# Performance work log

Measured on AMD Instinct MI355X. Metric: run time of the kernel, lower is better.

Reference implementation:

```python
import jax, jax.numpy as jnp
import numpy as np

C_S = 1024
H = 16
M = 1  # num_vector_messages
B, S = 2, 1024
SQRT3 = 3.0 ** 0.5
LN_EPS = 1e-5


def setup_inputs() -> dict:
    key = jax.random.key(0)
    ks = jax.random.split(key, 8)
    s = jax.random.normal(ks[0], (B, S, C_S), dtype=jnp.float32)
    # random proper-ish frames: orthonormalize random 3x3 via QR
    A = jax.random.normal(ks[1], (B, S, 3, 3), dtype=jnp.float32)
    rot, _ = jnp.linalg.qr(A)
    trans = jax.random.normal(ks[2], (B, S, 3), dtype=jnp.float32)
    affine_mask = jnp.ones((B, S), dtype=bool)
    sequence_id = jax.random.randint(ks[3], (B, S), 0, 4, dtype=jnp.int32)
    chain_id = jax.random.randint(ks[4], (B, S), 0, 4, dtype=jnp.int32)
    dim_proj = 4 * H * 3 + H * 3 * M
    ln_w = jnp.ones((C_S,), dtype=jnp.float32)
    w_proj = jax.random.normal(ks[5], (dim_proj, C_S), dtype=jnp.float32) / np.sqrt(C_S)
    w_out = jax.random.normal(ks[6], (C_S, H * 3 * M), dtype=jnp.float32) / np.sqrt(H * 3 * M)
    dist_scale = jnp.zeros((H,), dtype=jnp.float32)
    rot_scale = jnp.zeros((H,), dtype=jnp.float32)
    return {"s": s, "rot": rot, "trans": trans, "ln_w": ln_w, "w_proj": w_proj,
            "w_out": w_out, "dist_scale": dist_scale, "rot_scale": rot_scale,
            "affine_mask": affine_mask, "sequence_id": sequence_id, "chain_id": chain_id}


def reference(s, rot, trans, ln_w, w_proj, w_out, dist_scale, rot_scale,
              affine_mask, sequence_id, chain_id):
    b, n, c = s.shape
    h, m = H, M
    NEG = jnp.finfo(s.dtype).min
    # attention bias: 1.0 for same-sequence pairs, -inf for invalid frames / cross-chain
    seq_eq = (sequence_id[:, :, None] == sequence_id[:, None, :]).astype(s.dtype)
    bias = seq_eq[:, None]  # [b,1,s,s]
    bias = jnp.where(affine_mask[:, None, None, :], bias, NEG)
    chain_diff = chain_id[:, :, None] != chain_id[:, None, :]
    bias = jnp.where(chain_diff[:, None], NEG, bias)
    # LayerNorm (no bias)
    mu = jnp.mean(s, axis=-1, keepdims=True)
    var = jnp.var(s, axis=-1, keepdims=True)
    ns = (s - mu) / jnp.sqrt(var + LN_EPS) * ln_w
    p = jnp.einsum('bsc,dc->bsd', ns, w_proj)
    n_rot = h * 2 * 3 + h * 3 * m
    vec_rot = p[..., :n_rot].reshape(b, n, 2 * h + h * m, 3)
    vec_dist = p[..., n_rot:].reshape(b, n, 2 * h, 3)
    # rotate into global frame; dist vectors also translated
    rot_vecs = jnp.einsum('bsij,bshj->bshi', rot, vec_rot)
    q_rot, k_rot, value = rot_vecs[:, :, :h], rot_vecs[:, :, h:2 * h], rot_vecs[:, :, 2 * h:]
    dist_vecs = jnp.einsum('bsij,bshj->bshi', rot, vec_dist) + trans[:, :, None, :]
    q_dist, k_dist = dist_vecs[:, :, :h], dist_vecs[:, :, h:]
    # distance term [b,h,q,k]
    qd = q_dist.transpose(0, 2, 1, 3)  # b h s 3
    kd = k_dist.transpose(0, 2, 1, 3)
    diff = qd[:, :, :, None, :] - kd[:, :, None, :, :]
    distance_term = jnp.sqrt(jnp.sum(diff * diff, axis=-1)) / SQRT3
    rotation_term = jnp.einsum('bqhd,bkhd->bhqk', q_rot, k_rot) / SQRT3
    dw = jax.nn.softplus(dist_scale)[None, :, None, None]
    rw = jax.nn.softplus(rot_scale)[None, :, None, None]
    attn = rotation_term * rw - distance_term * dw + bias
    attn = jax.nn.softmax(attn, axis=-1)
    # value: b s (h m) 3 -> b h s (m 3)
    v = value.reshape(b, n, h, m, 3).transpose(0, 2, 1, 3, 4).reshape(b, h, n, m * 3)
    out = jnp.einsum('bhqk,bhkd->bhqd', attn, v)
    out = out.reshape(b, h, n, m, 3).transpose(0, 2, 1, 3, 4).reshape(b, n, h * m, 3)
    out = jnp.einsum('bsji,bshj->bshi', rot, out)  # inverse rotation R^T
    out = out.reshape(b, n, h * m * 3)
    out = jnp.where(affine_mask[..., None], out, 0.0)
    return jnp.einsum('bsd,cd->bsc', out, w_out)
```

## Files before the change

### kernel.cpp

```cpp
#include <hip/hip_runtime.h>
#include <math.h>

#define NB 2
#define NS 1024
#define NC 1024
#define NH 16
#define DIMP 240
#define KSPLIT 16
#define AKH 16

constexpr float INV_SQRT3 = 0.57735026919f;
constexpr float LOG2E     = 1.44269504089f;
constexpr float BIAS0     = -23.0831169f;
constexpr float BIAS1     = -21.6404252f;

__global__ __launch_bounds__(256) void pre_kernel(const float* __restrict__ s,
                                                  float2* __restrict__ stats,
                                                  const float* __restrict__ wp,
                                                  float* __restrict__ wt) {
    __shared__ float sh[64 * 61];
    int tid = threadIdx.x;
    if (blockIdx.x < NB * NS / 4) {
        int wave = tid >> 6, lane = tid & 63;
        int row = blockIdx.x * 4 + wave;
        const float4* sp = (const float4*)(s + (size_t)row * NC);
        float sum = 0.0f, sq = 0.0f;
        #pragma unroll
        for (int i = 0; i < 4; i++) {
            float4 v = sp[i * 64 + lane];
            sum += v.x + v.y + v.z + v.w;
            sq  += v.x * v.x + v.y * v.y + v.z * v.z + v.w * v.w;
        }
        #pragma unroll
        for (int off = 32; off; off >>= 1) {
            sum += __shfl_down(sum, off);
            sq  += __shfl_down(sq, off);
        }
        if (lane == 0) {
            float mu  = sum * (1.0f / NC);
            float var = sq * (1.0f / NC) - mu * mu;
            stats[row] = make_float2(mu, rsqrtf(var + 1e-5f));
        }
    } else {
        int bx = blockIdx.x - NB * NS / 4;
        int k0 = (bx & 15) * 64;
        int d0 = (bx >> 4) * 60;
        float (*T)[61] = (float (*)[61])sh;
        #pragma unroll
        for (int i = 0; i < 15; i++) {
            int idx = i * 256 + tid;
            int dd = idx >> 6, kk = idx & 63;
            T[kk][dd] = wp[(size_t)(d0 + dd) * NC + k0 + kk];
        }
        __syncthreads();
        #pragma unroll
        for (int i = 0; i < 15; i++) {
            int idx = i * 256 + tid;
            int kk = idx / 60, dd = idx % 60;
            wt[(size_t)(k0 + kk) * DIMP + d0 + dd] = T[kk][dd];
        }
    }
}

__global__ __launch_bounds__(256) void proj_kernel(const float* __restrict__ s,
                                                   const float2* __restrict__ stats,
                                                   const float* __restrict__ lnw,
                                                   const float* __restrict__ wt,
                                                   float* __restrict__ pp,
                                                   int use_atomic) {
    int tid = threadIdx.x;
    int wave = tid >> 6, lane = tid & 63;
    int row0 = blockIdx.x * 32;
    int ky = blockIdx.y;
    int k0 = ky * 64;

    __shared__ float A[32][64];
    #pragma unroll
    for (int i = 0; i < 2; i++) {
        int idx = tid + i * 256;
        int r = idx >> 4, c4 = idx & 15;
        float4 v = *(const float4*)(s + (size_t)(row0 + r) * NC + k0 + c4 * 4);
        float2 st = stats[row0 + r];
        float4 w = *(const float4*)(lnw + k0 + c4 * 4);
        float4 o;
        o.x = (v.x - st.x) * st.y * w.x;
        o.y = (v.y - st.x) * st.y * w.y;
        o.z = (v.z - st.x) * st.y * w.z;
        o.w = (v.w - st.x) * st.y * w.w;
        *(float4*)&A[r][c4 * 4] = o;
    }
    __syncthreads();

    int wr0 = wave * 8;
    int c0 = lane * 4;
    bool active = c0 < DIMP;
    int c0m = active ? c0 : (DIMP - 4);
    const float* wb = wt + (size_t)k0 * DIMP + c0m;

    float acc[8][4];
    #pragma unroll
    for (int r = 0; r < 8; r++)
        #pragma unroll
        for (int c = 0; c < 4; c++) acc[r][c] = 0.0f;

    float4 wa[4], wx[4];
    #pragma unroll
    for (int j = 0; j < 4; j++) wa[j] = *(const float4*)(wb + (size_t)j * DIMP);

    for (int g = 0; g < 16; g += 2) {
        #pragma unroll
        for (int j = 0; j < 4; j++)
            wx[j] = *(const float4*)(wb + (size_t)((g + 1) * 4 + j) * DIMP);
        #pragma unroll
        for (int r = 0; r < 8; r++) {
            float4 a4 = *(const float4*)&A[wr0 + r][g * 4];
            #pragma unroll
            for (int c = 0; c < 4; c++) {
                float* ac = &acc[r][c];
                *ac = fmaf(a4.x, ((const float*)&wa[0])[c], *ac);
                *ac = fmaf(a4.y, ((const float*)&wa[1])[c], *ac);
                *ac = fmaf(a4.z, ((const float*)&wa[2])[c], *ac);
                *ac = fmaf(a4.w, ((const float*)&wa[3])[c], *ac);
            }
        }
        int kn2 = (g + 2 < 16) ? (g + 2) * 4 : 0;
        #pragma unroll
        for (int j = 0; j < 4; j++)
            wa[j] = *(const float4*)(wb + (size_t)(kn2 + j) * DIMP);
        #pragma unroll
        for (int r = 0; r < 8; r++) {
            float4 a4 = *(const float4*)&A[wr0 + r][(g + 1) * 4];
            #pragma unroll
            for (int c = 0; c < 4; c++) {
                float* ac = &acc[r][c];
                *ac = fmaf(a4.x, ((const float*)&wx[0])[c], *ac);
                *ac = fmaf(a4.y, ((const float*)&wx[1])[c], *ac);
                *ac = fmaf(a4.z, ((const float*)&wx[2])[c], *ac);
                *ac = fmaf(a4.w, ((const float*)&wx[3])[c], *ac);
            }
        }
    }
    if (active) {
        if (use_atomic) {
            #pragma unroll
            for (int r = 0; r < 8; r++)
                #pragma unroll
                for (int c = 0; c < 4; c++)
                    atomicAdd(&pp[(size_t)(row0 + wr0 + r) * DIMP + c0 + c], acc[r][c]);
        } else {
            float* dst = pp + (size_t)ky * (NB * NS * DIMP);
            #pragma unroll
            for (int r = 0; r < 8; r++)
                *(float4*)(dst + (size_t)(row0 + wr0 + r) * DIMP + c0) =
                    make_float4(acc[r][0], acc[r][1], acc[r][2], acc[r][3]);
        }
    }
}

__global__ __launch_bounds__(256) void build_kernel(const float* __restrict__ pp, int nred,
                                                    const float* __restrict__ rot,
                                                    const float* __restrict__ trans,
                                                    const float* __restrict__ dist_scale,
                                                    const float* __restrict__ rot_scale,
                                                    const int* __restrict__ seq,
                                                    const int* __restrict__ chain,
                                                    const int* __restrict__ amask,
                                                    float4* __restrict__ qrb,
                                                    float4* __restrict__ qdb,
                                                    float4* __restrict__ kp) {
    int gid = blockIdx.x * 256 + threadIdx.x;
    if (gid >= NB * NS * 80) return;
    int j  = gid % 80;
    int bs = gid / 80;
    int b  = bs >> 10;
    int si = bs & 1023;
    int off = (j < 48) ? 3 * j : 144 + 3 * (j - 48);
    float vx = 0.0f, vy = 0.0f, vz = 0.0f;
    for (int ky = 0; ky < nred; ky++) {
        const float* pr = pp + (size_t)ky * (NB * NS * DIMP) + (size_t)bs * DIMP + off;
        vx += pr[0]; vy += pr[1]; vz += pr[2];
    }
    const float* R = rot + (size_t)bs * 9;
    float ox = R[0] * vx + R[1] * vy + R[2] * vz;
    float oy = R[3] * vx + R[4] * vy + R[5] * vz;
    float oz = R[6] * vx + R[7] * vy + R[8] * vz;
    if (j >= 48) {
        ox += trans[(size_t)bs * 3 + 0];
        oy += trans[(size_t)bs * 3 + 1];
        oz += trans[(size_t)bs * 3 + 2];
    }
    if (j < 16) {
        float sc = log1pf(__expf(rot_scale[j])) * INV_SQRT3 * LOG2E;
        qrb[(size_t)(b * NH + j) * NS + si] = make_float4(ox * sc, oy * sc, oz * sc, 0.0f);
    } else if (j < 32) {
        int h = j - 16;
        float ck = (float)chain[bs] + 1000.0f * (float)(1 - amask[bs]);
        kp[((size_t)(b * NH + h) * NS + si) * 3 + 0] = make_float4(ox, oy, oz, ck);
    } else if (j < 48) {
        int h = j - 32;
        kp[((size_t)(b * NH + h) * NS + si) * 3 + 2] = make_float4(ox, oy, oz, 0.0f);
    } else if (j < 64) {
        int h = j - 48;
        float sc = log1pf(__expf(dist_scale[h])) * INV_SQRT3 * LOG2E;
        qdb[(size_t)(b * NH + h) * NS + si] = make_float4(ox * sc, oy * sc, oz * sc, 0.0f);
    } else {
        int h = j - 64;
        float sc = log1pf(__expf(dist_scale[h])) * INV_SQRT3 * LOG2E;
        kp[((size_t)(b * NH + h) * NS + si) * 3 + 1] =
            make_float4(ox * sc, oy * sc, oz * sc, (float)seq[bs]);
    }
}

__global__ __launch_bounds__(256) void attn_kernel(
    const float4* __restrict__ qrb, const float4* __restrict__ qdb,
    const float4* __restrict__ kp,
    float4* __restrict__ pacc) {
    __shared__ float4 kS[192];
    int bx = blockIdx.x;
    int ks = bx & (AKH - 1), qc = (bx >> 4) & 3, bh = bx >> 6;
    int tid = threadIdx.x;
    int q = qc * 256 + tid;
    int base = bh * NS;
    const float4* kb = kp + (size_t)base * 3;

    if (tid < 192) kS[tid] = kb[(size_t)ks * 192 + tid];
    __syncthreads();

    float4 a = qrb[base + q];
    float4 d = qdb[base + q];
    float cq = kb[(size_t)q * 3 + 0].w;
    float sq = kb[(size_t)q * 3 + 1].w;

    float l = 0.0f, ax = 0.0f, ay = 0.0f, az = 0.0f;
    #pragma unroll 4
    for (int j = 0; j < 64; j++) {
        float4 f0 = kS[j * 3 + 0];
        float4 f1 = kS[j * 3 + 1];
        float4 f2 = kS[j * 3 + 2];
        float rt = fmaf(a.x, f0.x, fmaf(a.y, f0.y, a.z * f0.z));
        float dx = d.x - f1.x, dy = d.y - f1.y, dz = d.z - f1.z;
        float dist = __builtin_amdgcn_sqrtf(fmaf(dx, dx, fmaf(dy, dy, dz * dz)));
        float dc = f0.w - cq;
        float arg = fmaf(-100.0f, fabsf(dc), rt - dist) +
                    ((f1.w == sq) ? BIAS1 : BIAS0);
        float pw = exp2f(arg);
        l += pw;
        ax = fmaf(pw, f2.x, ax);
        ay = fmaf(pw, f2.y, ay);
        az = fmaf(pw, f2.z, az);
    }
    pacc[(size_t)ks * (32 * NS) + base + q] = make_float4(ax, ay, az, l);
}

__global__ __launch_bounds__(256) void finout_kernel(const float4* __restrict__ pacc,
                                                     const float4* __restrict__ kp,
                                                     const float* __restrict__ rot,
                                                     const float* __restrict__ wout,
                                                     float* __restrict__ out) {
    __shared__ float sm[8][48];
    int tid = threadIdx.x;
    int r0 = blockIdx.x * 8;
    if (tid < 128) {
        int r = tid & 7, h = tid >> 3;
        int bq = r0 + r;
        int b = bq >> 10, q = bq & 1023;
        int i = (b * NH + h) * NS + q;
        float sx = 0.0f, sy = 0.0f, sz = 0.0f, sw = 0.0f;
        #pragma unroll
        for (int j = 0; j < AKH; j++) {
            float4 t = pacc[(size_t)j * (NB * NH * NS) + i];
            sx += t.x; sy += t.y; sz += t.z; sw += t.w;
        }
        float inv = 1.0f / sw;
        float ox = sx * inv, oy = sy * inv, oz = sz * inv;
        const float* R = rot + (size_t)bq * 9;
        float wxv = R[0] * ox + R[3] * oy + R[6] * oz;
        float wyv = R[1] * ox + R[4] * oy + R[7] * oz;
        float wzv = R[2] * ox + R[5] * oy + R[8] * oz;
        float cq = kp[(size_t)i * 3].w;
        if (cq >= 500.0f) { wxv = 0; wyv = 0; wzv = 0; }
        sm[r][h * 3 + 0] = wxv;
        sm[r][h * 3 + 1] = wyv;
        sm[r][h * 3 + 2] = wzv;
    }
    __syncthreads();
    #pragma unroll 1
    for (int ch = 0; ch < 4; ch++) {
        int c = ch * 256 + tid;
        float w[48];
        #pragma unroll
        for (int d = 0; d < 48; d += 4) {
            float4 t = *(const float4*)(wout + (size_t)c * 48 + d);
            w[d] = t.x; w[d + 1] = t.y; w[d + 2] = t.z; w[d + 3] = t.w;
        }
        #pragma unroll 4
        for (int r = 0; r < 8; r++) {
            float acc = 0.0f;
            #pragma unroll
            for (int d = 0; d < 48; d++) acc = fmaf(w[d], sm[r][d], acc);
            out[(size_t)(r0 + r) * NC + c] = acc;
        }
    }
}

extern "C" void kernel_launch(void* const* d_in, const int* in_sizes, int n_in,
                              void* d_out, int out_size, void* d_ws, size_t ws_size,
                              hipStream_t stream) {
    const float* s     = (const float*)d_in[0];
    const float* rot   = (const float*)d_in[1];
    const float* trans = (const float*)d_in[2];
    const float* lnw   = (const float*)d_in[3];
    const float* wproj = (const float*)d_in[4];
    const float* wout  = (const float*)d_in[5];
    const float* dsc   = (const float*)d_in[6];
    const float* rsc   = (const float*)d_in[7];
    const int* amask   = (const int*)d_in[8];
    const int* seq     = (const int*)d_in[9];
    const int* chain   = (const int*)d_in[10];
    float* out = (float*)d_out;

    float2* stats = (float2*)d_ws;
    float4* qrb = (float4*)((float*)d_ws + 4096);
    float4* qdb = qrb + (size_t)NB * NH * NS;
    float4* kpk = qdb + (size_t)NB * NH * NS;
    float* pp = (float*)(kpk + (size_t)3 * NB * NH * NS);
    float* wt = (float*)qrb;
    float4* pacc = (float4*)pp;

    size_t need = ((char*)(pp + (size_t)KSPLIT * NB * NS * DIMP)) - (char*)d_ws;
    int use_atomic = (ws_size < need) ? 1 : 0;

    pre_kernel<<<NB * NS / 4 + 64, 256, 0, stream>>>(s, stats, wproj, wt);
    if (use_atomic) {
        hipMemsetAsync(pp, 0, (size_t)NB * NS * DIMP * sizeof(float), stream);
        proj_kernel<<<dim3(64, KSPLIT), 256, 0, stream>>>(s, stats, lnw, wt, pp, 1);
        build_kernel<<<(NB * NS * 80 + 255) / 256, 256, 0, stream>>>(pp, 1, rot, trans, dsc, rsc,
                                                                     seq, chain, amask, qrb, qdb, kpk);
    } else {
        proj_kernel<<<dim3(64, KSPLIT), 256, 0, stream>>>(s, stats, lnw, wt, pp, 0);
        build_kernel<<<(NB * NS * 80 + 255) / 256, 256, 0, stream>>>(pp, KSPLIT, rot, trans, dsc, rsc,
                                                                     seq, chain, amask, qrb, qdb, kpk);
    }
    attn_kernel<<<NB * NH * 4 * AKH, 256, 0, stream>>>(qrb, qdb, kpk, pacc);
    finout_kernel<<<NB * NS / 8, 256, 0, stream>>>(pacc, kpk, rot, wout, out);
}
```

Before: 150.2 us.

## Halve split-K factors and pre-transpose output weights for coalesced loads

Both the projection GEMM and the attention kernel now use 8 splits instead of 16. Each proj block handles 128 input channels and each attention block handles 128 keys, which halves the partial sums written and later reduced. A new pre_kernel section transposes w_out into a float4-interleaved layout, so finout loads its weights coalesced across threads instead of as per-thread contiguous 48-float rows. The attention kernel also issues its q loads before the barrier so they overlap the shared-memory fill. The trade-off is fewer blocks in flight, which lowers parallelism and the ability to hide latency on a large GPU.

```diff
diff --git a/kernel.cpp b/kernel.cpp
--- a/kernel.cpp
+++ b/kernel.cpp
@@ -6,8 +6,8 @@
 #define NC 1024
 #define NH 16
 #define DIMP 240
-#define KSPLIT 16
-#define AKH 16
+#define KSPLIT 8
+#define AKH 8
 
 constexpr float INV_SQRT3 = 0.57735026919f;
 constexpr float LOG2E     = 1.44269504089f;
@@ -17,7 +17,9 @@
 __global__ __launch_bounds__(256) void pre_kernel(const float* __restrict__ s,
                                                   float2* __restrict__ stats,
                                                   const float* __restrict__ wp,
-                                                  float* __restrict__ wt) {
+                                                  float* __restrict__ wt,
+                                                  const float* __restrict__ wout,
+                                                  float4* __restrict__ wtp) {
     __shared__ float sh[64 * 61];
     int tid = threadIdx.x;
     if (blockIdx.x < NB * NS / 4) {
@@ -41,7 +43,7 @@
             float var = sq * (1.0f / NC) - mu * mu;
             stats[row] = make_float2(mu, rsqrtf(var + 1e-5f));
         }
-    } else {
+    } else if (blockIdx.x < NB * NS / 4 + 64) {
         int bx = blockIdx.x - NB * NS / 4;
         int k0 = (bx & 15) * 64;
         int d0 = (bx >> 4) * 60;
@@ -58,6 +60,14 @@
             int idx = i * 256 + tid;
             int kk = idx / 60, dd = idx % 60;
             wt[(size_t)(k0 + kk) * DIMP + d0 + dd] = T[kk][dd];
+        }
+    } else {
+        int d4 = blockIdx.x - (NB * NS / 4 + 64);
+        const float4* wof = (const float4*)wout;
+        #pragma unroll
+        for (int i = 0; i < 4; i++) {
+            int c = i * 256 + tid;
+            wtp[(size_t)d4 * 1024 + c] = wof[(size_t)c * 12 + d4];
         }
     }
 }
@@ -72,13 +82,13 @@
     int wave = tid >> 6, lane = tid & 63;
     int row0 = blockIdx.x * 32;
     int ky = blockIdx.y;
-    int k0 = ky * 64;
-
-    __shared__ float A[32][64];
+    int k0 = ky * 128;
+
+    __shared__ float A[32][128];
     #pragma unroll
-    for (int i = 0; i < 2; i++) {
+    for (int i = 0; i < 4; i++) {
         int idx = tid + i * 256;
-        int r = idx >> 4, c4 = idx & 15;
+        int r = idx >> 5, c4 = idx & 31;
         float4 v = *(const float4*)(s + (size_t)(row0 + r) * NC + k0 + c4 * 4);
         float2 st = stats[row0 + r];
         float4 w = *(const float4*)(lnw + k0 + c4 * 4);
@@ -107,7 +117,7 @@
     #pragma unroll
     for (int j = 0; j < 4; j++) wa[j] = *(const float4*)(wb + (size_t)j * DIMP);
 
-    for (int g = 0; g < 16; g += 2) {
+    for (int g = 0; g < 32; g += 2) {
         #pragma unroll
         for (int j = 0; j < 4; j++)
             wx[j] = *(const float4*)(wb + (size_t)((g + 1) * 4 + j) * DIMP);
@@ -123,7 +133,7 @@
                 *ac = fmaf(a4.w, ((const float*)&wa[3])[c], *ac);
             }
         }
-        int kn2 = (g + 2 < 16) ? (g + 2) * 4 : 0;
+        int kn2 = (g + 2 < 32) ? (g + 2) * 4 : 0;
         #pragma unroll
         for (int j = 0; j < 4; j++)
             wa[j] = *(const float4*)(wb + (size_t)(kn2 + j) * DIMP);
@@ -215,25 +225,25 @@
     const float4* __restrict__ qrb, const float4* __restrict__ qdb,
     const float4* __restrict__ kp,
     float4* __restrict__ pacc) {
-    __shared__ float4 kS[192];
+    __shared__ float4 kS[384];
     int bx = blockIdx.x;
-    int ks = bx & (AKH - 1), qc = (bx >> 4) & 3, bh = bx >> 6;
+    int ks = bx & (AKH - 1), qc = (bx >> 3) & 3, bh = bx >> 5;
     int tid = threadIdx.x;
     int q = qc * 256 + tid;
     int base = bh * NS;
     const float4* kb = kp + (size_t)base * 3;
 
-    if (tid < 192) kS[tid] = kb[(size_t)ks * 192 + tid];
-    __syncthreads();
+    for (int i = tid; i < 384; i += 256) kS[i] = kb[(size_t)ks * 384 + i];
 
     float4 a = qrb[base + q];
     float4 d = qdb[base + q];
     float cq = kb[(size_t)q * 3 + 0].w;
     float sq = kb[(size_t)q * 3 + 1].w;
+    __syncthreads();
 
     float l = 0.0f, ax = 0.0f, ay = 0.0f, az = 0.0f;
     #pragma unroll 4
-    for (int j = 0; j < 64; j++) {
+    for (int j = 0; j < 128; j++) {
         float4 f0 = kS[j * 3 + 0];
         float4 f1 = kS[j * 3 + 1];
         float4 f2 = kS[j * 3 + 2];
@@ -249,13 +259,13 @@
         ay = fmaf(pw, f2.y, ay);
         az = fmaf(pw, f2.z, az);
     }
-    pacc[(size_t)ks * (32 * NS) + base + q] = make_float4(ax, ay, az, l);
+    pacc[(size_t)ks * (NB * NH * NS) + base + q] = make_float4(ax, ay, az, l);
 }
 
 __global__ __launch_bounds__(256) void finout_kernel(const float4* __restrict__ pacc,
                                                      const float4* __restrict__ kp,
                                                      const float* __restrict__ rot,
-                                                     const float* __restrict__ wout,
+                                                     const float4* __restrict__ wtp,
                                                      float* __restrict__ out) {
     __shared__ float sm[8][48];
     int tid = threadIdx.x;
@@ -287,17 +297,20 @@
     #pragma unroll 1
     for (int ch = 0; ch < 4; ch++) {
         int c = ch * 256 + tid;
-        float w[48];
-        #pragma unroll
-        for (int d = 0; d < 48; d += 4) {
-            float4 t = *(const float4*)(wout + (size_t)c * 48 + d);
-            w[d] = t.x; w[d + 1] = t.y; w[d + 2] = t.z; w[d + 3] = t.w;
-        }
+        float4 wreg[12];
+        #pragma unroll
+        for (int d4 = 0; d4 < 12; d4++) wreg[d4] = wtp[(size_t)d4 * 1024 + c];
         #pragma unroll 4
         for (int r = 0; r < 8; r++) {
             float acc = 0.0f;
             #pragma unroll
-            for (int d = 0; d < 48; d++) acc = fmaf(w[d], sm[r][d], acc);
+            for (int d4 = 0; d4 < 12; d4++) {
+                float4 w4 = wreg[d4];
+                acc = fmaf(w4.x, sm[r][d4 * 4 + 0], acc);
+                acc = fmaf(w4.y, sm[r][d4 * 4 + 1], acc);
+                acc = fmaf(w4.z, sm[r][d4 * 4 + 2], acc);
+                acc = fmaf(w4.w, sm[r][d4 * 4 + 3], acc);
+            }
             out[(size_t)(r0 + r) * NC + c] = acc;
         }
     }
@@ -324,13 +337,14 @@
     float4* qdb = qrb + (size_t)NB * NH * NS;
     float4* kpk = qdb + (size_t)NB * NH * NS;
     float* pp = (float*)(kpk + (size_t)3 * NB * NH * NS);
+    float4* wtp = (float4*)(pp + (size_t)KSPLIT * NB * NS * DIMP);
     float* wt = (float*)qrb;
     float4* pacc = (float4*)pp;
 
-    size_t need = ((char*)(pp + (size_t)KSPLIT * NB * NS * DIMP)) - (char*)d_ws;
+    size_t need = ((char*)(wtp + 12 * 1024)) - (char*)d_ws;
     int use_atomic = (ws_size < need) ? 1 : 0;
 
-    pre_kernel<<<NB * NS / 4 + 64, 256, 0, stream>>>(s, stats, wproj, wt);
+    pre_kernel<<<NB * NS / 4 + 64 + 12, 256, 0, stream>>>(s, stats, wproj, wt, wout, wtp);
     if (use_atomic) {
         hipMemsetAsync(pp, 0, (size_t)NB * NS * DIMP * sizeof(float), stream);
         proj_kernel<<<dim3(64, KSPLIT), 256, 0, stream>>>(s, stats, lnw, wt, pp, 1);
@@ -342,5 +356,5 @@
                                                                      seq, chain, amask, qrb, qdb, kpk);
     }
     attn_kernel<<<NB * NH * 4 * AKH, 256, 0, stream>>>(qrb, qdb, kpk, pacc);
-    finout_kernel<<<NB * NS / 8, 256, 0, stream>>>(pacc, kpk, rot, wout, out);
-}
+    finout_kernel<<<NB * NS / 8, 256, 0, stream>>>(pacc, kpk, rot, wtp, out);
+}
```

New measurement: 156.8 us. 1.04x slower.
